# Kernel tuning notes

Measured on AMD Instinct MI355X. Metric: run time of the kernel, lower is better.

The kernel has to match this reference:

```python
import jax, jax.numpy as jnp
import numpy as np

B = 2
N = 300000
C_IN = 2
PC = (-75.2, -75.2, 75.2, 75.2)
BEV = 0.8
GRID = int(round((PC[2] - PC[0]) / BEV))  # 188
CH = 256


def setup_inputs() -> dict:
    key = jax.random.key(0)
    ks = jax.random.split(key, 8)
    xy = jax.random.uniform(ks[0], (N, 2), minval=PC[0], maxval=PC[2], dtype=jnp.float32)
    z = jax.random.uniform(ks[1], (N, 1), minval=-2.0, maxval=4.0, dtype=jnp.float32)
    xyz = jnp.concatenate([xy, z], axis=-1)
    xyz_batch_cnt = jnp.full((B,), N // B, dtype=jnp.int32)
    pt_features = jax.random.normal(ks[2], (N, C_IN), dtype=jnp.float32)
    mlp_w = jax.random.normal(ks[3], (6 + C_IN, CH), dtype=jnp.float32) * 0.1
    mlp_g = jnp.ones((CH,), jnp.float32)
    mlp_b = jnp.zeros((CH,), jnp.float32)
    conv4_w = jax.random.normal(ks[4], (5, 3, 3, CH, CH), dtype=jnp.float32) * 0.02
    conv4_g = jnp.ones((5, CH), jnp.float32)
    conv4_b = jnp.zeros((5, CH), jnp.float32)
    conv5_w = jax.random.normal(ks[5], (5, 3, 3, CH, CH), dtype=jnp.float32) * 0.02
    conv5_g = jnp.ones((5, CH), jnp.float32)
    conv5_b = jnp.zeros((5, CH), jnp.float32)
    return dict(xyz=xyz, pt_features=pt_features, xyz_batch_cnt=xyz_batch_cnt,
                mlp_w=mlp_w, mlp_g=mlp_g, mlp_b=mlp_b,
                conv4_w=conv4_w, conv4_g=conv4_g, conv4_b=conv4_b,
                conv5_w=conv5_w, conv5_g=conv5_g, conv5_b=conv5_b)


def _conv(x, w, stride=1):
    # NHWC input, HWIO kernel, torch padding=1
    return jax.lax.conv_general_dilated(x, w, (stride, stride), [(1, 1), (1, 1)],
                                        dimension_numbers=("NHWC", "HWIO", "NHWC"))


def _bn(x, g, b):
    # eval-mode BatchNorm folded into per-channel affine
    return x * g + b


def _forward(xyz, pt_features, xyz_batch_cnt, mlp_w, mlp_g, mlp_b,
             conv4_w, conv4_g, conv4_b, conv5_w, conv5_g, conv5_b):
    n = xyz.shape[0]
    batch_idx = jnp.repeat(jnp.arange(B, dtype=jnp.int32), xyz_batch_cnt, total_repeat_length=n)
    ix = jnp.clip(jnp.floor((xyz[:, 0] - PC[0]) / BEV).astype(jnp.int32), 0, GRID - 1)
    iy = jnp.clip(jnp.floor((xyz[:, 1] - PC[1]) / BEV).astype(jnp.int32), 0, GRID - 1)
    cx = PC[0] + (ix.astype(xyz.dtype) + 0.5) * BEV
    cy = PC[1] + (iy.astype(xyz.dtype) + 0.5) * BEV
    # 6 geometric features (xyz + offsets to pillar center) + raw point features
    feat = jnp.concatenate([xyz,
                            (xyz[:, 0] - cx)[:, None],
                            (xyz[:, 1] - cy)[:, None],
                            xyz[:, 2:3],
                            pt_features], axis=-1)  # [N, 8]
    h = jax.nn.relu(_bn(feat @ mlp_w, mlp_g, mlp_b))  # [N, 256]
    flat = (batch_idx * GRID + iy) * GRID + ix  # [N]
    grid = jnp.full((B * GRID * GRID, CH), -jnp.inf, h.dtype).at[flat].max(h)
    occ = jnp.zeros((B * GRID * GRID, 1), h.dtype).at[flat].set(1.0)
    x = jnp.where(occ > 0, grid, 0.0).reshape(B, GRID, GRID, CH)
    mask = occ.reshape(B, GRID, GRID, 1)
    relu = jax.nn.relu
    # Sparse2DBasicBlockV (submanifold convs == dense conv on zero-padded grid + active-site mask)
    x0 = mask * relu(_bn(_conv(x, conv4_w[0]), conv4_g[0], conv4_b[0]))
    out = mask * relu(_bn(_conv(x0, conv4_w[1]), conv4_g[1], conv4_b[1]))
    out = mask * _bn(_conv(out, conv4_w[2]), conv4_g[2], conv4_b[2])
    x1 = relu(out + x0)
    # Sparse2DBasicBlock
    out = mask * relu(_bn(_conv(x1, conv4_w[3]), conv4_g[3], conv4_b[3]))
    out = mask * _bn(_conv(out, conv4_w[4]), conv4_g[4], conv4_b[4])
    x_conv4 = relu(out + x1)  # [B, 188, 188, 256]
    # conv5: strided dense conv + 2 Dense2DBasicBlocks
    y = relu(_bn(_conv(x_conv4, conv5_w[0], stride=2), conv5_g[0], conv5_b[0]))  # [B, 94, 94, 256]
    for i in (1, 3):
        out = relu(_bn(_conv(y, conv5_w[i]), conv5_g[i], conv5_b[i]))
        out = _bn(_conv(out, conv5_w[i + 1]), conv5_g[i + 1], conv5_b[i + 1])
        y = relu(out + y)
    return (jnp.transpose(x_conv4, (0, 3, 1, 2)), jnp.transpose(y, (0, 3, 1, 2)))


def reference(xyz, pt_features, xyz_batch_cnt, mlp_w, mlp_g, mlp_b,
              conv4_w, conv4_g, conv4_b, conv5_w, conv5_g, conv5_b):
    return _forward(xyz, pt_features, xyz_batch_cnt, mlp_w, mlp_g, mlp_b,
                    conv4_w, conv4_g, conv4_b, conv5_w, conv5_g, conv5_b)
```

## Files before the change

### kernel.cpp

```cpp
#include <hip/hip_runtime.h>
#include <hip/hip_bf16.h>


typedef __attribute__((ext_vector_type(8))) short bf16x8;
typedef __attribute__((ext_vector_type(4))) float f32x4;
typedef unsigned short u16;

#define GLD16(g, l)                                                   \
    __builtin_amdgcn_global_load_lds(                                 \
        (const __attribute__((address_space(1))) void*)(g),           \
        (__attribute__((address_space(3))) void*)(l), 16, 0, 0)

__device__ __forceinline__ u16 f2b(float f) {
    unsigned u = __float_as_uint(f);
    u += 0x7fffu + ((u >> 16) & 1u);
    return (u16)(u >> 16);
}
__device__ __forceinline__ float b2f(u16 h) {
    return __uint_as_float(((unsigned)h) << 16);
}

__global__ __launch_bounds__(256) void bin_kernel(
    const float* __restrict__ xyz, const int* __restrict__ cnt,
    int* __restrict__ pcnt, int* __restrict__ plist, int N) {
    int i = blockIdx.x * 256 + threadIdx.x;
    if (i >= N) return;
    float x = xyz[3 * i], y = xyz[3 * i + 1];
    int b = (i < cnt[0]) ? 0 : 1;
    int ix = (int)floorf((x + 75.2f) / 0.8f);
    int iy = (int)floorf((y + 75.2f) / 0.8f);
    ix = min(max(ix, 0), 187);
    iy = min(max(iy, 0), 187);
    int flat = (b * 188 + iy) * 188 + ix;
    int slot = atomicAdd(pcnt + flat, 1);
    if (slot < 32) plist[flat * 32 + slot] = i;
}

__global__ __launch_bounds__(256) void pillar_kernel(
    const float* __restrict__ xyz, const float* __restrict__ ptf,
    const float* __restrict__ mw, const float* __restrict__ mg,
    const float* __restrict__ mb, const int* __restrict__ pcnt,
    const int* __restrict__ plist, u16* __restrict__ out,
    float* __restrict__ occ) {
    const int lane = threadIdx.x & 63, wid = threadIdx.x >> 6;
    const int p = blockIdx.x * 4 + wid;
    const int n = min(pcnt[p], 32);
    const int c = lane * 4;
    float m0 = 0.f, m1 = 0.f, m2 = 0.f, m3 = 0.f;
    if (n > 0) {
        const int ix = p % 188;
        const int iy = (p / 188) % 188;
        const float cx = -75.2f + ((float)ix + 0.5f) * 0.8f;
        const float cy = -75.2f + ((float)iy + 0.5f) * 0.8f;
        float4 w[8];
#pragma unroll
        for (int k = 0; k < 8; k++) w[k] = *(const float4*)(mw + k * 256 + c);
        for (int t = 0; t < n; t++) {
            int i = __builtin_amdgcn_readfirstlane(plist[p * 32 + t]);
            float x = xyz[3 * i], y = xyz[3 * i + 1], z = xyz[3 * i + 2];
            float f0 = ptf[2 * i], f1 = ptf[2 * i + 1];
            const float f[8] = {x, y, z, x - cx, y - cy, z, f0, f1};
            float s0 = 0.f, s1 = 0.f, s2 = 0.f, s3 = 0.f;
#pragma unroll
            for (int k = 0; k < 8; k++) {
                s0 = fmaf(f[k], w[k].x, s0);
                s1 = fmaf(f[k], w[k].y, s1);
                s2 = fmaf(f[k], w[k].z, s2);
                s3 = fmaf(f[k], w[k].w, s3);
            }
            float4 g4 = *(const float4*)(mg + c);
            float4 b4 = *(const float4*)(mb + c);
            m0 = fmaxf(m0, fmaxf(s0 * g4.x + b4.x, 0.f));
            m1 = fmaxf(m1, fmaxf(s1 * g4.y + b4.y, 0.f));
            m2 = fmaxf(m2, fmaxf(s2 * g4.z + b4.z, 0.f));
            m3 = fmaxf(m3, fmaxf(s3 * g4.w + b4.w, 0.f));
        }
    }
    unsigned lo = (unsigned)f2b(m0) | ((unsigned)f2b(m1) << 16);
    unsigned hi = (unsigned)f2b(m2) | ((unsigned)f2b(m3) << 16);
    *(uint2*)(out + (size_t)p * 256 + c) = make_uint2(lo, hi);
    if (lane == 0) occ[p] = (n > 0) ? 1.f : 0.f;
}

__global__ void cvt_weights_kernel(const float* __restrict__ w4,
                                   const float* __restrict__ w5,
                                   u16* __restrict__ wt4,
                                   u16* __restrict__ wt5) {
    int bid = blockIdx.x;
    int mat = bid >> 4;
    int tile = bid & 15;
    int tr = tile >> 2, tc = tile & 3;
    const float* src = (mat < 45) ? (w4 + (size_t)mat * 65536)
                                  : (w5 + (size_t)(mat - 45) * 65536);
    u16* dst = (mat < 45) ? (wt4 + (size_t)mat * 65536)
                          : (wt5 + (size_t)(mat - 45) * 65536);
    __shared__ u16 sm[64][65];
    int tx = threadIdx.x & 63, ty = threadIdx.x >> 6;
#pragma unroll
    for (int k = 0; k < 64; k += 4) {
        int c = tr * 64 + ty + k;
        int n = tc * 64 + tx;
        sm[tx][ty + k] = f2b(src[c * 256 + n]);
    }
    __syncthreads();
#pragma unroll
    for (int k = 0; k < 64; k += 4) {
        int n = tc * 64 + ty + k;
        int c = tr * 64 + tx;
        dst[n * 256 + c] = sm[ty + k][tx];
    }
}

template <int STRIDE, bool HAS_MASK, bool HAS_RES, bool HAS_F32OUT>
__global__ __launch_bounds__(256) void conv3x3_kernel(
    const u16* __restrict__ in, const u16* __restrict__ wt,
    const u16* __restrict__ zeros, const float* __restrict__ gamma,
    const float* __restrict__ beta, const float* __restrict__ mask,
    const u16* __restrict__ res, u16* __restrict__ outb,
    float* __restrict__ outf, int Hin, int Win, int Hout, int Wout, int Bn) {
    const int M = Bn * Hout * Wout;
    const int HWo = Hout * Wout;
    const int HWi = Hin * Win;
    const int tid = threadIdx.x;
    const int lane = tid & 63, wid = tid >> 6;
    const int wr = wid >> 1, wc = wid & 1;
    const int nwg = gridDim.x;
    const int q = nwg >> 3, r = nwg & 7;
    const int xc = blockIdx.x & 7, jj = blockIdx.x >> 3;
    const int wg = (xc < r ? xc * (q + 1) : r * (q + 1) + (xc - r) * q) + jj;
    const int m0 = (wg >> 1) * 128;
    const int n0 = (wg & 1) * 128;

    __shared__ u16 SMEM[40960];
    const int lrow = lane >> 3;
    const int csw = (((lane & 7) ^ (lrow & 7)) << 3);

    int ppy[4], ppx[4], ppb[4];
    bool ppo[4];
#pragma unroll
    for (int j = 0; j < 4; j++) {
        int gp = m0 + wid * 32 + j * 8 + lrow;
        ppo[j] = gp < M;
        int g2 = ppo[j] ? gp : 0;
        int b = g2 / HWo;
        int rr = g2 - b * HWo;
        ppy[j] = rr / Wout;
        ppx[j] = rr - ppy[j] * Wout;
        ppb[j] = b;
    }
    int bofs[4];
#pragma unroll
    for (int j = 0; j < 4; j++)
        bofs[j] = (n0 + wid * 32 + j * 8 + lrow) * 256 + csw;

#define MKPTR(dst, T)                                                         \
    do {                                                                      \
        int dy_ = (T) / 3 - 1, dx_ = (T) % 3 - 1;                             \
        _Pragma("unroll") for (int j = 0; j < 4; j++) {                       \
            int sy_ = ppy[j] * STRIDE + dy_;                                  \
            int sx_ = ppx[j] * STRIDE + dx_;                                  \
            bool ok_ = ppo[j] && sy_ >= 0 && sy_ < Hin && sx_ >= 0 &&         \
                       sx_ < Win;                                             \
            long long off_ =                                                  \
                ((long long)ppb[j] * HWi + (long long)sy_ * Win + sx_) * 256; \
            dst[j] = ok_ ? in + off_ + csw : zeros + csw;                     \
        }                                                                     \
    } while (0)

#define ISSUE_A(APTR, KC, SLOT)                                               \
    do {                                                                      \
        u16* dA_ = SMEM + (SLOT)*8192;                                        \
        _Pragma("unroll") for (int j = 0; j < 4; j++) {                       \
            GLD16(APTR[j] + (KC)*64, dA_ + (wid * 32 + j * 8) * 64);          \
        }                                                                     \
    } while (0)

#define ISSUE_B(T, KC, SLOT)                                                  \
    do {                                                                      \
        u16* dB_ = SMEM + 24576 + (SLOT)*8192;                                \
        _Pragma("unroll") for (int j = 0; j < 4; j++) {                       \
            GLD16(wt + (T)*65536 + bofs[j] + (KC)*64,                         \
                  dB_ + (wid * 32 + j * 8) * 64);                             \
        }                                                                     \
    } while (0)

    f32x4 acc[4][4];
#pragma unroll
    for (int m = 0; m < 4; m++)
#pragma unroll
        for (int n = 0; n < 4; n++) acc[m][n] = (f32x4)0.f;

    const u16* aptrc[4];
    const u16* aptrn[4];
    MKPTR(aptrc, 0);
    ISSUE_A(aptrc, 0, 0);
    ISSUE_B(0, 0, 0);
    ISSUE_A(aptrc, 1, 1);

    const int rA = lane & 15;
    const int kb = (lane >> 4) * 8;
    const int xk = (rA & 7) << 3;
    int b0 = 0;

#pragma unroll 1
    for (int t = 0; t < 9; t++) {
        MKPTR(aptrn, t + 1);
#pragma unroll
        for (int kc = 0; kc < 4; kc++) {
            const int s = t * 4 + kc;
            int ib = b0 + kc;
            if (ib >= 3) ib -= 3;
            if (s < 35) {
                asm volatile("s_waitcnt vmcnt(4)" ::: "memory");
            } else {
                asm volatile("s_waitcnt vmcnt(0)" ::: "memory");
            }
            __builtin_amdgcn_sched_barrier(0);
            __builtin_amdgcn_s_barrier();
            __builtin_amdgcn_sched_barrier(0);
            if (s < 35) {
                if (kc < 3) {
                    ISSUE_B(t, kc + 1, (kc + 1) & 1);
                } else {
                    ISSUE_B(t + 1, 0, 0);
                }
            }
            if (s < 34) {
                int ia = ib + 2;
                if (ia >= 3) ia -= 3;
                if (kc < 2) {
                    ISSUE_A(aptrc, kc + 2, ia);
                } else {
                    ISSUE_A(aptrn, kc - 2, ia);
                }
            }
            __builtin_amdgcn_sched_barrier(0);
            const u16* Ar = SMEM + ib * 8192;
            const u16* Br = SMEM + 24576 + (kc & 1) * 8192;
#pragma unroll
            for (int kh = 0; kh < 2; kh++) {
                bf16x8 af[4], bfr[4];
#pragma unroll
                for (int m = 0; m < 4; m++)
                    af[m] = *(const bf16x8*)(Ar + (wr * 64 + m * 16 + rA) * 64 +
                                             ((kh * 32 + kb) ^ xk));
#pragma unroll
                for (int n = 0; n < 4; n++)
                    bfr[n] = *(const bf16x8*)(Br + (wc * 64 + n * 16 + rA) * 64 +
                                              ((kh * 32 + kb) ^ xk));
                __builtin_amdgcn_s_setprio(1);
#pragma unroll
                for (int m = 0; m < 4; m++)
#pragma unroll
                    for (int n = 0; n < 4; n++)
                        acc[m][n] = __builtin_amdgcn_mfma_f32_16x16x32_bf16(
                            af[m], bfr[n], acc[m][n], 0, 0, 0);
                __builtin_amdgcn_s_setprio(0);
            }
        }
#pragma unroll
        for (int j = 0; j < 4; j++) aptrc[j] = aptrn[j];
        b0 = (b0 == 2) ? 0 : b0 + 1;
    }

    __syncthreads();
    float* ep = (float*)SMEM + wid * 2112;
    const int cb = n0 + wc * 64;
    float gms[4], bts[4];
#pragma unroll
    for (int n = 0; n < 4; n++) {
        gms[n] = gamma[cb + n * 16 + rA];
        bts[n] = beta[cb + n * 16 + rA];
    }
#pragma unroll
    for (int half = 0; half < 2; half++) {
#pragma unroll
        for (int m2 = 0; m2 < 2; m2++) {
            const int m = half * 2 + m2;
            const int lrb = m2 * 16 + ((lane >> 4) << 2);
            const int gpb = m0 + wr * 64 + half * 32 + lrb;
#pragma unroll
            for (int rr = 0; rr < 4; rr++) {
                float mk = 1.f;
                if (HAS_MASK) mk = (gpb + rr < M) ? mask[gpb + rr] : 0.f;
#pragma unroll
                for (int n = 0; n < 4; n++) {
                    float v = acc[m][n][rr] * gms[n] + bts[n];
                    if (HAS_MASK) v *= mk;
                    ep[(lrb + rr) * 66 + n * 16 + rA] = v;
                }
            }
        }
#pragma unroll
        for (int i = 0; i < 8; i++) {
            const int lr = i * 4 + (lane >> 4);
            const int gp = m0 + wr * 64 + half * 32 + lr;
            f32x4 v = *(const f32x4*)(ep + lr * 66 + rA * 4);
            if (HAS_RES && gp < M) {
                uint2 rv = *(const uint2*)(res + (size_t)gp * 256 + cb + rA * 4);
                v[0] += b2f((u16)(rv.x & 0xffff));
                v[1] += b2f((u16)(rv.x >> 16));
                v[2] += b2f((u16)(rv.y & 0xffff));
                v[3] += b2f((u16)(rv.y >> 16));
            }
            v[0] = fmaxf(v[0], 0.f);
            v[1] = fmaxf(v[1], 0.f);
            v[2] = fmaxf(v[2], 0.f);
            v[3] = fmaxf(v[3], 0.f);
            if (HAS_F32OUT) *(f32x4*)(ep + lr * 66 + rA * 4) = v;
            if (gp < M) {
                unsigned lo = (unsigned)f2b(v[0]) | ((unsigned)f2b(v[1]) << 16);
                unsigned hi = (unsigned)f2b(v[2]) | ((unsigned)f2b(v[3]) << 16);
                *(uint2*)(outb + (size_t)gp * 256 + cb + rA * 4) =
                    make_uint2(lo, hi);
            }
        }
        if (HAS_F32OUT) {
#pragma unroll
            for (int i = 0; i < 16; i++) {
                const int lc = i * 4 + (lane >> 4);
                const int p0 = rA * 2;
                const int gp0 = m0 + wr * 64 + half * 32 + p0;
                if (gp0 < M) {
                    float v0 = ep[p0 * 66 + lc];
                    float v1 = ep[(p0 + 1) * 66 + lc];
                    int b = gp0 / HWo;
                    int rr = gp0 - b * HWo;
                    const int ch = cb + lc;
                    float* o = outf + ((size_t)(b * 256 + ch)) * HWo + rr;
                    *(float2*)o = make_float2(v0, v1);
                }
            }
        }
    }
#undef MKPTR
#undef ISSUE_A
#undef ISSUE_B
}

extern "C" void kernel_launch(void* const* d_in, const int* in_sizes, int n_in,
                              void* d_out, int out_size, void* d_ws,
                              size_t ws_size, hipStream_t stream) {
    const float* xyz = (const float*)d_in[0];
    const float* ptf = (const float*)d_in[1];
    const int* cnt = (const int*)d_in[2];
    const float* mw = (const float*)d_in[3];
    const float* mg = (const float*)d_in[4];
    const float* mb = (const float*)d_in[5];
    const float* c4w = (const float*)d_in[6];
    const float* c4g = (const float*)d_in[7];
    const float* c4b = (const float*)d_in[8];
    const float* c5w = (const float*)d_in[9];
    const float* c5g = (const float*)d_in[10];
    const float* c5b = (const float*)d_in[11];
    const int N = in_sizes[0] / 3;

    char* ws = (char*)d_ws;
    int* pcnt = (int*)ws;
    u16* zeros = (u16*)(ws + 282752);
    float* occ = (float*)(ws + 283264);
    int* plist = (int*)(ws + 566016);
    u16* wt4 = (u16*)(ws + 9614080);
    u16* wt5 = (u16*)(ws + 15512320);
    u16* bufA = (u16*)(ws + 21410560);
    u16* bufB = (u16*)(ws + 57602816);
    u16* bufC = (u16*)(ws + 93795072);

    float* outXC4 = (float*)d_out;
    float* outY = ((float*)d_out) + 18096128;

    const int M188 = 2 * 188 * 188;
    const int M94 = 2 * 94 * 94;

    hipMemsetAsync(ws, 0, 283264, stream);
    cvt_weights_kernel<<<90 * 16, 256, 0, stream>>>(c4w, c5w, wt4, wt5);
    bin_kernel<<<(N + 255) / 256, 256, 0, stream>>>(xyz, cnt, pcnt, plist, N);
    pillar_kernel<<<M188 / 4, 256, 0, stream>>>(xyz, ptf, mw, mg, mb, pcnt,
                                                plist, bufA, occ);

    dim3 g188(2 * ((M188 + 127) / 128)), g94(2 * ((M94 + 127) / 128));
    const size_t WL = 9 * 65536;

    conv3x3_kernel<1, true, false, false><<<g188, 256, 0, stream>>>(
        bufA, wt4 + 0 * WL, zeros, c4g + 0, c4b + 0, occ, nullptr, bufB,
        nullptr, 188, 188, 188, 188, 2);
    conv3x3_kernel<1, true, false, false><<<g188, 256, 0, stream>>>(
        bufB, wt4 + 1 * WL, zeros, c4g + 256, c4b + 256, occ, nullptr, bufC,
        nullptr, 188, 188, 188, 188, 2);
    conv3x3_kernel<1, true, true, false><<<g188, 256, 0, stream>>>(
        bufC, wt4 + 2 * WL, zeros, c4g + 512, c4b + 512, occ, bufB, bufA,
        nullptr, 188, 188, 188, 188, 2);
    conv3x3_kernel<1, true, false, false><<<g188, 256, 0, stream>>>(
        bufA, wt4 + 3 * WL, zeros, c4g + 768, c4b + 768, occ, nullptr, bufC,
        nullptr, 188, 188, 188, 188, 2);
    conv3x3_kernel<1, true, true, true><<<g188, 256, 0, stream>>>(
        bufC, wt4 + 4 * WL, zeros, c4g + 1024, c4b + 1024, occ, bufA, bufB,
        outXC4, 188, 188, 188, 188, 2);

    conv3x3_kernel<2, false, false, false><<<g94, 256, 0, stream>>>(
        bufB, wt5 + 0 * WL, zeros, c5g + 0, c5b + 0, nullptr, nullptr, bufA,
        nullptr, 188, 188, 94, 94, 2);
    conv3x3_kernel<1, false, false, false><<<g94, 256, 0, stream>>>(
        bufA, wt5 + 1 * WL, zeros, c5g + 256, c5b + 256, nullptr, nullptr,
        bufC, nullptr, 94, 94, 94, 94, 2);
    conv3x3_kernel<1, false, true, false><<<g94, 256, 0, stream>>>(
        bufC, wt5 + 2 * WL, zeros, c5g + 512, c5b + 512, nullptr, bufA, bufB,
        nullptr, 94, 94, 94, 94, 2);
    conv3x3_kernel<1, false, false, false><<<g94, 256, 0, stream>>>(
        bufB, wt5 + 3 * WL, zeros, c5g + 768, c5b + 768, nullptr, nullptr,
        bufC, nullptr, 94, 94, 94, 94, 2);
    conv3x3_kernel<1, false, true, true><<<g94, 256, 0, stream>>>(
        bufC, wt5 + 4 * WL, zeros, c5g + 1024, c5b + 1024, nullptr, bufB,
        bufA, outY, 94, 94, 94, 94, 2);
}
```

Measured before the change: 847.7 us.

## Load conv weights straight into registers in MFMA fragment layout, drop LDS B tiles

Weights are now pre-permuted by the conversion kernel into per-lane MFMA fragment order, so each wave loads its B operand with direct 16-byte global loads into double-buffered registers instead of staging through LDS. This cuts the LDS footprint from 80KB to 48KB, and launch bounds now request two blocks per SM for higher occupancy. It also removes the LDS reads for B. The costs are more VGPRs (16 bf16x8 fragments), a looser vmcnt wait, and possible spills under the occupancy cap.

```diff
diff --git a/kernel.cpp b/kernel.cpp
--- a/kernel.cpp
+++ b/kernel.cpp
@@ -10,6 +10,8 @@
     __builtin_amdgcn_global_load_lds(                                 \
         (const __attribute__((address_space(1))) void*)(g),           \
         (__attribute__((address_space(3))) void*)(l), 16, 0, 0)
+
+#define SB0 __builtin_amdgcn_sched_barrier(0)
 
 __device__ __forceinline__ u16 f2b(float f) {
     unsigned u = __float_as_uint(f);
@@ -82,37 +84,32 @@
     if (lane == 0) occ[p] = (n > 0) ? 1.f : 0.f;
 }
 
-__global__ void cvt_weights_kernel(const float* __restrict__ w4,
-                                   const float* __restrict__ w5,
-                                   u16* __restrict__ wt4,
-                                   u16* __restrict__ wt5) {
-    int bid = blockIdx.x;
-    int mat = bid >> 4;
-    int tile = bid & 15;
-    int tr = tile >> 2, tc = tile & 3;
+__global__ __launch_bounds__(256) void cvt_weights_kernel(
+    const float* __restrict__ w4, const float* __restrict__ w5,
+    u16* __restrict__ wt4, u16* __restrict__ wt5) {
+    int g = blockIdx.x * 256 + threadIdx.x;
+    int mat = g >> 13;
+    int r = g & 8191;
+    int nb = r >> 11;
+    int kc = (r >> 9) & 3;
+    int kh = (r >> 8) & 1;
+    int nf = (r >> 6) & 3;
+    int lane = r & 63;
+    int c0 = kc * 64 + kh * 32 + (lane >> 4) * 8;
+    int n = nb * 64 + nf * 16 + (lane & 15);
     const float* src = (mat < 45) ? (w4 + (size_t)mat * 65536)
                                   : (w5 + (size_t)(mat - 45) * 65536);
-    u16* dst = (mat < 45) ? (wt4 + (size_t)mat * 65536)
-                          : (wt5 + (size_t)(mat - 45) * 65536);
-    __shared__ u16 sm[64][65];
-    int tx = threadIdx.x & 63, ty = threadIdx.x >> 6;
-#pragma unroll
-    for (int k = 0; k < 64; k += 4) {
-        int c = tr * 64 + ty + k;
-        int n = tc * 64 + tx;
-        sm[tx][ty + k] = f2b(src[c * 256 + n]);
-    }
-    __syncthreads();
-#pragma unroll
-    for (int k = 0; k < 64; k += 4) {
-        int n = tc * 64 + ty + k;
-        int c = tr * 64 + tx;
-        dst[n * 256 + c] = sm[ty + k][tx];
-    }
+    u16* dst = ((mat < 45) ? (wt4 + (size_t)mat * 65536)
+                           : (wt5 + (size_t)(mat - 45) * 65536)) +
+               (size_t)r * 8;
+    u16 v[8];
+#pragma unroll
+    for (int e = 0; e < 8; e++) v[e] = f2b(src[(c0 + e) * 256 + n]);
+    *(uint4*)dst = *(const uint4*)v;
 }
 
 template <int STRIDE, bool HAS_MASK, bool HAS_RES, bool HAS_F32OUT>
-__global__ __launch_bounds__(256) void conv3x3_kernel(
+__global__ __launch_bounds__(256, 2) void conv3x3_kernel(
     const u16* __restrict__ in, const u16* __restrict__ wt,
     const u16* __restrict__ zeros, const float* __restrict__ gamma,
     const float* __restrict__ beta, const float* __restrict__ mask,
@@ -131,7 +128,7 @@
     const int m0 = (wg >> 1) * 128;
     const int n0 = (wg & 1) * 128;
 
-    __shared__ u16 SMEM[40960];
+    __shared__ u16 SMEM[24576];
     const int lrow = lane >> 3;
     const int csw = (((lane & 7) ^ (lrow & 7)) << 3);
 
@@ -148,10 +145,8 @@
         ppx[j] = rr - ppy[j] * Wout;
         ppb[j] = b;
     }
-    int bofs[4];
-#pragma unroll
-    for (int j = 0; j < 4; j++)
-        bofs[j] = (n0 + wid * 32 + j * 8 + lrow) * 256 + csw;
+    const int nb = (n0 >> 6) + wc;
+    const u16* wb = wt + (size_t)nb * 16384 + lane * 8;
 
 #define MKPTR(dst, T)                                                         \
     do {                                                                      \
@@ -175,31 +170,57 @@
         }                                                                     \
     } while (0)
 
-#define ISSUE_B(T, KC, SLOT)                                                  \
-    do {                                                                      \
-        u16* dB_ = SMEM + 24576 + (SLOT)*8192;                                \
-        _Pragma("unroll") for (int j = 0; j < 4; j++) {                       \
-            GLD16(wt + (T)*65536 + bofs[j] + (KC)*64,                         \
-                  dB_ + (wid * 32 + j * 8) * 64);                             \
-        }                                                                     \
-    } while (0)
-
     f32x4 acc[4][4];
 #pragma unroll
     for (int m = 0; m < 4; m++)
 #pragma unroll
         for (int n = 0; n < 4; n++) acc[m][n] = (f32x4)0.f;
+
+    const int rA = lane & 15;
+    const int kb = (lane >> 4) * 8;
+    const int xk = (rA & 7) << 3;
+
+    bf16x8 bS0[8], bS1[8];
+    auto loadB = [&](bf16x8(&dst)[8], int tt, int kk) {
+        const u16* base = wb + tt * 65536 + kk * 4096;
+#pragma unroll
+        for (int nf = 0; nf < 4; nf++)
+#pragma unroll
+            for (int kh = 0; kh < 2; kh++)
+                dst[nf * 2 + kh] =
+                    *(const bf16x8*)(base + kh * 2048 + nf * 512);
+    };
+    auto stepc = [&](const u16* Ar, const bf16x8(&bu)[8]) {
+#pragma unroll
+        for (int kh = 0; kh < 2; kh++) {
+            bf16x8 af[4];
+#pragma unroll
+            for (int m = 0; m < 4; m++)
+                af[m] = *(const bf16x8*)(Ar + (wr * 64 + m * 16 + rA) * 64 +
+                                         ((kh * 32 + kb) ^ xk));
+            __builtin_amdgcn_s_setprio(1);
+#pragma unroll
+            for (int m = 0; m < 4; m++)
+#pragma unroll
+                for (int n = 0; n < 4; n++)
+                    acc[m][n] = __builtin_amdgcn_mfma_f32_16x16x32_bf16(
+                        af[m], bu[n * 2 + kh], acc[m][n], 0, 0, 0);
+            __builtin_amdgcn_s_setprio(0);
+        }
+    };
 
     const u16* aptrc[4];
     const u16* aptrn[4];
     MKPTR(aptrc, 0);
     ISSUE_A(aptrc, 0, 0);
-    ISSUE_B(0, 0, 0);
+    SB0;
+    loadB(bS0, 0, 0);
+    SB0;
     ISSUE_A(aptrc, 1, 1);
-
-    const int rA = lane & 15;
-    const int kb = (lane >> 4) * 8;
-    const int xk = (rA & 7) << 3;
+    SB0;
+    loadB(bS1, 0, 1);
+    SB0;
+
     int b0 = 0;
 
 #pragma unroll 1
@@ -211,20 +232,13 @@
             int ib = b0 + kc;
             if (ib >= 3) ib -= 3;
             if (s < 35) {
-                asm volatile("s_waitcnt vmcnt(4)" ::: "memory");
+                asm volatile("s_waitcnt vmcnt(12)" ::: "memory");
             } else {
                 asm volatile("s_waitcnt vmcnt(0)" ::: "memory");
             }
-            __builtin_amdgcn_sched_barrier(0);
+            SB0;
             __builtin_amdgcn_s_barrier();
-            __builtin_amdgcn_sched_barrier(0);
-            if (s < 35) {
-                if (kc < 3) {
-                    ISSUE_B(t, kc + 1, (kc + 1) & 1);
-                } else {
-                    ISSUE_B(t + 1, 0, 0);
-                }
-            }
+            SB0;
             if (s < 34) {
                 int ia = ib + 2;
                 if (ia >= 3) ia -= 3;
@@ -234,29 +248,24 @@
                     ISSUE_A(aptrn, kc - 2, ia);
                 }
             }
-            __builtin_amdgcn_sched_barrier(0);
+            SB0;
             const u16* Ar = SMEM + ib * 8192;
-            const u16* Br = SMEM + 24576 + (kc & 1) * 8192;
-#pragma unroll
-            for (int kh = 0; kh < 2; kh++) {
-                bf16x8 af[4], bfr[4];
-#pragma unroll
-                for (int m = 0; m < 4; m++)
-                    af[m] = *(const bf16x8*)(Ar + (wr * 64 + m * 16 + rA) * 64 +
-                                             ((kh * 32 + kb) ^ xk));
-#pragma unroll
-                for (int n = 0; n < 4; n++)
-                    bfr[n] = *(const bf16x8*)(Br + (wc * 64 + n * 16 + rA) * 64 +
-                                              ((kh * 32 + kb) ^ xk));
-                __builtin_amdgcn_s_setprio(1);
-#pragma unroll
-                for (int m = 0; m < 4; m++)
-#pragma unroll
-                    for (int n = 0; n < 4; n++)
-                        acc[m][n] = __builtin_amdgcn_mfma_f32_16x16x32_bf16(
-                            af[m], bfr[n], acc[m][n], 0, 0, 0);
-                __builtin_amdgcn_s_setprio(0);
-            }
+            if (kc & 1) {
+                stepc(Ar, bS1);
+            } else {
+                stepc(Ar, bS0);
+            }
+            SB0;
+            if (s < 34) {
+                const int tB = (kc < 2) ? t : t + 1;
+                const int kB = (kc < 2) ? kc + 2 : kc - 2;
+                if (kc & 1) {
+                    loadB(bS1, tB, kB);
+                } else {
+                    loadB(bS0, tB, kB);
+                }
+            }
+            SB0;
         }
 #pragma unroll
         for (int j = 0; j < 4; j++) aptrc[j] = aptrn[j];
@@ -335,7 +344,6 @@
     }
 #undef MKPTR
 #undef ISSUE_A
-#undef ISSUE_B
 }
 
 extern "C" void kernel_launch(void* const* d_in, const int* in_sizes, int n_in,
@@ -373,7 +381,7 @@
     const int M94 = 2 * 94 * 94;
 
     hipMemsetAsync(ws, 0, 283264, stream);
-    cvt_weights_kernel<<<90 * 16, 256, 0, stream>>>(c4w, c5w, wt4, wt5);
+    cvt_weights_kernel<<<2880, 256, 0, stream>>>(c4w, c5w, wt4, wt5);
     bin_kernel<<<(N + 255) / 256, 256, 0, stream>>>(xyz, cnt, pcnt, plist, N);
     pillar_kernel<<<M188 / 4, 256, 0, stream>>>(xyz, ptf, mw, mg, mb, pcnt,
                                                 plist, bufA, occ);
```

Result: slower. 903.9 us (+6.6%).
